# Kernel optimization log

Measured on AMD Instinct MI355X. Metric: run time of the kernel, lower is better.

## Reference

```python
import jax, jax.numpy as jnp
import numpy as np


def setup_inputs() -> dict:
    key = jax.random.key(0)
    k1, k2, k3, k4 = jax.random.split(key, 4)
    N, M, D = 4096, 4096, 1024
    H = jax.random.normal(k1, (N, D), dtype=jnp.float32)
    K = jax.random.normal(k2, (M, D), dtype=jnp.float32)
    V = jax.random.normal(k3, (M, D), dtype=jnp.float32)
    attn_mask = jax.random.uniform(k4, (N, M), dtype=jnp.float32)
    return {"H": H, "K": K, "V": V, "attn_mask": attn_mask}


def reference(H, K, V, attn_mask):
    # scores: [N, M] = H @ K^T, scaled by sqrt(d)
    d = H.shape[1]
    scores = jnp.matmul(H, K.T) / jnp.sqrt(jnp.asarray(d, dtype=H.dtype))
    # double softmax with elementwise mask multiply in between
    probs = jax.nn.softmax(jax.nn.softmax(scores, axis=1) * attn_mask, axis=1)
    return jnp.matmul(probs, V)
```

## Files before the change

kernel.cpp:

```cpp
#include <hip/hip_runtime.h>
#include <cstdint>

typedef unsigned short u16;
typedef __bf16 bf16x8 __attribute__((ext_vector_type(8)));
typedef float f32x4 __attribute__((ext_vector_type(4)));
typedef unsigned int u32x4 __attribute__((ext_vector_type(4)));

__device__ __forceinline__ float bf2f(u16 h) {
  union { unsigned int u; float f; } v; v.u = ((unsigned int)h) << 16; return v.f;
}
__device__ __forceinline__ u16 f2bf(float f) {
  union { float f; unsigned int u; } v; v.f = f;
  unsigned int u = v.u;
  return (u16)((u + 0x7FFFu + ((u >> 16) & 1u)) >> 16);
}

__device__ __forceinline__ void ld_lds16(const void* g, void* l) {
  __builtin_amdgcn_global_load_lds(
      (const __attribute__((address_space(1))) unsigned int*)g,
      (__attribute__((address_space(3))) unsigned int*)l, 16, 0, 0);
}

__global__ __launch_bounds__(512, 2) void gemm1_kernel(
    const u16* __restrict__ A, const u16* __restrict__ B,
    u16* __restrict__ S, int ldA, int ldB, int ldC)
{
  __shared__ __align__(16) u16 smem[65536];

  const int tid  = threadIdx.x;
  const int lane = tid & 63;
  const int w    = tid >> 6;
  const int wr   = w >> 2;
  const int wc   = w & 3;
  const int quad = lane >> 4;
  const int cIn  = lane & 15;
  const int lrow   = lane >> 3;
  const int gchunk = (lane & 7) ^ lrow;

  const int flat = blockIdx.x;
  const int xcd  = flat & 7;
  const int i    = flat >> 3;
  const int rowT = (xcd >> 1) * 4 + (i & 3);
  const int colT = (xcd & 1) * 8 + (i >> 2);
  const int rowBlk = rowT * 256;
  const int colBlk = colT * 256;

  f32x4 acc[8][4];
  #pragma unroll
  for (int a = 0; a < 8; ++a)
    #pragma unroll
    for (int b = 0; b < 4; ++b) acc[a][b] = {0.f, 0.f, 0.f, 0.f};

  auto stageA = [&](int buf, int kt2) {
    #pragma unroll
    for (int l = 0; l < 4; ++l) {
      const u16* ga = A + (size_t)(rowBlk + l * 64 + w * 8 + lrow) * ldA
                        + kt2 * 64 + gchunk * 8;
      ld_lds16(ga, &smem[buf * 16384 + l * 4096 + w * 512]);
    }
  };
  auto stageB = [&](int buf, int kt2) {
    #pragma unroll
    for (int l = 0; l < 4; ++l) {
      const u16* gb = B + (size_t)(colBlk + l * 64 + w * 8 + lrow) * ldB
                        + kt2 * 64 + gchunk * 8;
      ld_lds16(gb, &smem[32768 + buf * 16384 + l * 4096 + w * 512]);
    }
  };

  stageA(0, 0);
  stageB(0, 0);
  __syncthreads();

  for (int kt = 0; kt < 16; ++kt) {
    const int cur = kt & 1;
    const int aBase = cur * 16384;
    const int bBase = 32768 + cur * 16384;

    bf16x8 bf[4][2];
    #pragma unroll
    for (int q = 0; q < 4; ++q) {
      if (q == 0) {
        if (kt + 1 < 16) stageA(cur ^ 1, kt + 1);
        #pragma unroll
        for (int ni = 0; ni < 4; ++ni)
          #pragma unroll
          for (int ks = 0; ks < 2; ++ks) {
            int row = wc * 64 + ni * 16 + cIn;
            int ch  = (ks * 4 + quad) ^ (row & 7);
            bf[ni][ks] = *(const bf16x8*)&smem[bBase + row * 64 + ch * 8];
          }
      }
      if (q == 1 && kt + 1 < 16) stageB(cur ^ 1, kt + 1);

      bf16x8 af[2][2];
      #pragma unroll
      for (int m = 0; m < 2; ++m)
        #pragma unroll
        for (int ks = 0; ks < 2; ++ks) {
          int row = wr * 128 + (q * 2 + m) * 16 + cIn;
          int ch  = (ks * 4 + quad) ^ (row & 7);
          af[m][ks] = *(const bf16x8*)&smem[aBase + row * 64 + ch * 8];
        }

      __builtin_amdgcn_s_barrier();
      asm volatile("s_waitcnt lgkmcnt(0)" ::: "memory");
      __builtin_amdgcn_sched_barrier(0);
      __builtin_amdgcn_s_setprio(1);
      #pragma unroll
      for (int m = 0; m < 2; ++m)
        #pragma unroll
        for (int ni = 0; ni < 4; ++ni)
          #pragma unroll
          for (int ks = 0; ks < 2; ++ks)
            acc[q * 2 + m][ni] = __builtin_amdgcn_mfma_f32_16x16x32_bf16(
                af[m][ks], bf[ni][ks], acc[q * 2 + m][ni], 0, 0, 0);
      __builtin_amdgcn_s_setprio(0);
      __builtin_amdgcn_sched_barrier(0);
      if (q < 3) __builtin_amdgcn_s_barrier();
    }
    __syncthreads();
  }

  const float scale = 0.03125f;
  u16* epi = smem;
  #pragma unroll
  for (int R = 0; R < 4; ++R) {
    #pragma unroll
    for (int m01 = 0; m01 < 2; ++m01) {
      int mi = R * 2 + m01;
      #pragma unroll
      for (int ni = 0; ni < 4; ++ni) {
        int col = wc * 64 + ni * 16 + cIn;
        #pragma unroll
        for (int r = 0; r < 4; ++r) {
          int er = wr * 32 + m01 * 16 + quad * 4 + r;
          epi[er * 264 + col] = f2bf(acc[mi][ni][r] * scale);
        }
      }
    }
    __syncthreads();
    #pragma unroll
    for (int it = 0; it < 4; ++it) {
      int idx = it * 512 + tid;
      int er  = idx >> 5;
      int c8  = idx & 31;
      int grow = rowBlk + (er >> 5) * 128 + (R * 2 + ((er >> 4) & 1)) * 16 + (er & 15);
      u32x4 v = *(const u32x4*)&epi[er * 264 + c8 * 8];
      *(u32x4*)&S[(size_t)grow * ldC + colBlk + c8 * 8] = v;
    }
    __syncthreads();
  }
}

__global__ __launch_bounds__(256) void gemm2_kernel(
    const u16* __restrict__ A, const u16* __restrict__ B,
    float* __restrict__ Out, const float* __restrict__ L2,
    int ldA, int ldB, int ldC)
{
  __shared__ __align__(16) u16 smem[49152];

  const int tid  = threadIdx.x;
  const int lane = tid & 63;
  const int w    = tid >> 6;
  const int wrow = w >> 1;
  const int wcol = w & 1;
  const int quad = lane >> 4;
  const int cIn  = lane & 15;
  const int lrow   = lane >> 3;
  const int gchunk = (lane & 7) ^ lrow;

  const int flat = blockIdx.x;
  const int xcd  = flat & 7;
  const int i    = flat >> 3;
  const int rowBlk = (xcd * 4 + (i & 3)) * 128;
  const int colBlk = (i >> 2) * 128;

  f32x4 acc[4][4];
  #pragma unroll
  for (int a = 0; a < 4; ++a)
    #pragma unroll
    for (int b = 0; b < 4; ++b) acc[a][b] = {0.f, 0.f, 0.f, 0.f};

  auto stage = [&](int buf, int kt) {
    int kk = kt * 64;
    #pragma unroll
    for (int t = 0; t < 4; ++t) {
      int rg = w * 4 + t;
      const u16* ga = A + (size_t)(rowBlk + rg * 8 + lrow) * ldA + kk + gchunk * 8;
      ld_lds16(ga, &smem[buf * 8192 + rg * 512]);
      const u16* gb = B + (size_t)(colBlk + rg * 8 + lrow) * ldB + kk + gchunk * 8;
      ld_lds16(gb, &smem[24576 + buf * 8192 + rg * 512]);
    }
  };

  stage(0, 0);
  stage(1, 1);

  int cur = 0;
  for (int kt = 0; kt < 64; ++kt) {
    if (kt < 63) asm volatile("s_waitcnt vmcnt(8)" ::: "memory");
    else         asm volatile("s_waitcnt vmcnt(0)" ::: "memory");
    __builtin_amdgcn_s_barrier();
    __builtin_amdgcn_sched_barrier(0);

    if (kt + 2 < 64) {
      int nb = cur + 2; if (nb >= 3) nb -= 3;
      stage(nb, kt + 2);
    }

    const int aBase = cur * 8192;
    const int bBase = 24576 + cur * 8192;
    #pragma unroll
    for (int ks = 0; ks < 2; ++ks) {
      bf16x8 af[4], bfr[4];
      #pragma unroll
      for (int mi = 0; mi < 4; ++mi) {
        int row = wrow * 64 + mi * 16 + cIn;
        int ch  = (ks * 4 + quad) ^ (row & 7);
        af[mi]  = *(const bf16x8*)&smem[aBase + row * 64 + ch * 8];
      }
      #pragma unroll
      for (int ni = 0; ni < 4; ++ni) {
        int row = wcol * 64 + ni * 16 + cIn;
        int ch  = (ks * 4 + quad) ^ (row & 7);
        bfr[ni] = *(const bf16x8*)&smem[bBase + row * 64 + ch * 8];
      }
      #pragma unroll
      for (int mi = 0; mi < 4; ++mi)
        #pragma unroll
        for (int ni = 0; ni < 4; ++ni)
          acc[mi][ni] = __builtin_amdgcn_mfma_f32_16x16x32_bf16(
              af[mi], bfr[ni], acc[mi][ni], 0, 0, 0);
    }

    cur = (cur + 1 == 3) ? 0 : cur + 1;
  }

  #pragma unroll
  for (int mi = 0; mi < 4; ++mi) {
    #pragma unroll
    for (int r = 0; r < 4; ++r) {
      int row   = rowBlk + wrow * 64 + mi * 16 + quad * 4 + r;
      float inv = 1.0f / L2[row];
      #pragma unroll
      for (int ni = 0; ni < 4; ++ni) {
        int col = colBlk + wcol * 64 + ni * 16 + cIn;
        __builtin_nontemporal_store(acc[mi][ni][r] * inv,
                                    &Out[(size_t)row * ldC + col]);
      }
    }
  }
}

__global__ __launch_bounds__(256) void prep_kernel(
    const float* __restrict__ H, const float* __restrict__ Kin,
    const float* __restrict__ V, u16* __restrict__ Hb, u16* __restrict__ Kb,
    u16* __restrict__ Vt)
{
  int b = blockIdx.x;
  if (b < 8192) {
    const float* src = (b < 4096) ? H : Kin;
    u16* dst = (b < 4096) ? Hb : Kb;
    int i = (b & 4095) * 256 + threadIdx.x;
    f32x4 v = __builtin_nontemporal_load(&((const f32x4*)src)[i]);
    ushort4 o;
    o.x = f2bf(v.x); o.y = f2bf(v.y); o.z = f2bf(v.z); o.w = f2bf(v.w);
    ((ushort4*)dst)[i] = o;
  } else {
    __shared__ float tile[32][33];
    b -= 8192;
    int c0 = (b & 31) * 32;
    int r0 = (b >> 5) * 32;
    int tx = threadIdx.x & 31, ty = threadIdx.x >> 5;
    #pragma unroll
    for (int s = 0; s < 32; s += 8)
      tile[ty + s][tx] = __builtin_nontemporal_load(
          &V[(size_t)(r0 + ty + s) * 1024 + c0 + tx]);
    __syncthreads();
    #pragma unroll
    for (int s = 0; s < 32; s += 8)
      Vt[(size_t)(c0 + ty + s) * 4096 + r0 + tx] = f2bf(tile[tx][ty + s]);
  }
}

__global__ __launch_bounds__(256) void softmax2_kernel(
    u16* __restrict__ S, const float* __restrict__ mask,
    float* __restrict__ L2, int M)
{
  int row = blockIdx.x;
  u16* srow = S + (size_t)row * M;
  const float* mrow = mask + (size_t)row * M;
  const int base = threadIdx.x * 16;

  u16 sl[16];
  *(uint4*)(sl)     = *(const uint4*)(srow + base);
  *(uint4*)(sl + 8) = *(const uint4*)(srow + base + 8);

  float e[16];
  float s1 = 0.f;
  #pragma unroll
  for (int j = 0; j < 16; ++j) { e[j] = __expf(bf2f(sl[j])); s1 += e[j]; }

  __shared__ float wred[8];
  #pragma unroll
  for (int m = 1; m < 64; m <<= 1) s1 += __shfl_xor(s1, m, 64);
  if ((threadIdx.x & 63) == 0) wred[threadIdx.x >> 6] = s1;
  __syncthreads();
  float inv = 1.0f / (wred[0] + wred[1] + wred[2] + wred[3]);

  float mv[16];
  #pragma unroll
  for (int q = 0; q < 4; ++q) {
    f32x4 m4 = __builtin_nontemporal_load((const f32x4*)(mrow + base + q * 4));
    mv[q * 4 + 0] = m4.x; mv[q * 4 + 1] = m4.y;
    mv[q * 4 + 2] = m4.z; mv[q * 4 + 3] = m4.w;
  }

  float lsum = 0.f;
  #pragma unroll
  for (int j = 0; j < 16; ++j) {
    float p = __expf(e[j] * inv * mv[j]);
    lsum += p;
    sl[j] = f2bf(p);
  }
  *(uint4*)(srow + base)     = *(uint4*)(sl);
  *(uint4*)(srow + base + 8) = *(uint4*)(sl + 8);

  #pragma unroll
  for (int m = 1; m < 64; m <<= 1) lsum += __shfl_xor(lsum, m, 64);
  if ((threadIdx.x & 63) == 0) wred[4 + (threadIdx.x >> 6)] = lsum;
  __syncthreads();
  if (threadIdx.x == 0) L2[row] = wred[4] + wred[5] + wred[6] + wred[7];
}

extern "C" void kernel_launch(void* const* d_in, const int* in_sizes, int n_in,
                              void* d_out, int out_size, void* d_ws, size_t ws_size,
                              hipStream_t stream) {
  const float* H    = (const float*)d_in[0];
  const float* Kin  = (const float*)d_in[1];
  const float* V    = (const float*)d_in[2];
  const float* mask = (const float*)d_in[3];
  float* out = (float*)d_out;

  const int N = 4096, M = 4096, D = 1024;

  char* ws = (char*)d_ws;
  u16*   Hb = (u16*)(ws);
  u16*   Kb = (u16*)(ws + (8ull << 20));
  u16*   Vt = (u16*)(ws + (16ull << 20));
  u16*   S  = (u16*)(ws + (24ull << 20));
  float* L2 = (float*)(ws + (56ull << 20));

  prep_kernel<<<dim3(12288), dim3(256), 0, stream>>>(H, Kin, V, Hb, Kb, Vt);

  gemm1_kernel<<<dim3(256), dim3(512), 0, stream>>>(Hb, Kb, S, D, D, M);

  softmax2_kernel<<<dim3(N), dim3(256), 0, stream>>>(S, mask, L2, M);

  gemm2_kernel<<<dim3(256), dim3(256), 0, stream>>>(S, Vt, out, L2, M, M, D);
}
```

Baseline: 234.6 us.

## Split gemm2 K-loop across wave pairs with LDS reduction, 512 threads

gemm2 now runs 8 waves per block instead of 4. Each pair of waves splits the 64-wide K tile in half, and the two partial accumulators are combined through LDS in the epilogue. Global-to-LDS staging is spread over twice as many threads, and the MFMA section is raised in priority with s_setprio. The aim is more latency hiding and more MFMA issue per CU for the small grid of 256 blocks, at the cost of an extra LDS reduction pass and barriers.

```diff
diff --git a/kernel.cpp b/kernel.cpp
--- a/kernel.cpp
+++ b/kernel.cpp
@@ -153,7 +153,7 @@
   }
 }
 
-__global__ __launch_bounds__(256) void gemm2_kernel(
+__global__ __launch_bounds__(512, 2) void gemm2_kernel(
     const u16* __restrict__ A, const u16* __restrict__ B,
     float* __restrict__ Out, const float* __restrict__ L2,
     int ldA, int ldB, int ldC)
@@ -163,8 +163,9 @@
   const int tid  = threadIdx.x;
   const int lane = tid & 63;
   const int w    = tid >> 6;
-  const int wrow = w >> 1;
-  const int wcol = w & 1;
+  const int wk   = w & 1;
+  const int wrow = (w >> 1) & 1;
+  const int wcol = (w >> 2) & 1;
   const int quad = lane >> 4;
   const int cIn  = lane & 15;
   const int lrow   = lane >> 3;
@@ -185,8 +186,8 @@
   auto stage = [&](int buf, int kt) {
     int kk = kt * 64;
     #pragma unroll
-    for (int t = 0; t < 4; ++t) {
-      int rg = w * 4 + t;
+    for (int t = 0; t < 2; ++t) {
+      int rg = w * 2 + t;
       const u16* ga = A + (size_t)(rowBlk + rg * 8 + lrow) * ldA + kk + gchunk * 8;
       ld_lds16(ga, &smem[buf * 8192 + rg * 512]);
       const u16* gb = B + (size_t)(colBlk + rg * 8 + lrow) * ldB + kk + gchunk * 8;
@@ -199,7 +200,7 @@
 
   int cur = 0;
   for (int kt = 0; kt < 64; ++kt) {
-    if (kt < 63) asm volatile("s_waitcnt vmcnt(8)" ::: "memory");
+    if (kt < 63) asm volatile("s_waitcnt vmcnt(4)" ::: "memory");
     else         asm volatile("s_waitcnt vmcnt(0)" ::: "memory");
     __builtin_amdgcn_s_barrier();
     __builtin_amdgcn_sched_barrier(0);
@@ -211,43 +212,58 @@
 
     const int aBase = cur * 8192;
     const int bBase = 24576 + cur * 8192;
-    #pragma unroll
-    for (int ks = 0; ks < 2; ++ks) {
-      bf16x8 af[4], bfr[4];
-      #pragma unroll
-      for (int mi = 0; mi < 4; ++mi) {
-        int row = wrow * 64 + mi * 16 + cIn;
-        int ch  = (ks * 4 + quad) ^ (row & 7);
-        af[mi]  = *(const bf16x8*)&smem[aBase + row * 64 + ch * 8];
-      }
-      #pragma unroll
-      for (int ni = 0; ni < 4; ++ni) {
-        int row = wcol * 64 + ni * 16 + cIn;
-        int ch  = (ks * 4 + quad) ^ (row & 7);
-        bfr[ni] = *(const bf16x8*)&smem[bBase + row * 64 + ch * 8];
-      }
-      #pragma unroll
-      for (int mi = 0; mi < 4; ++mi)
-        #pragma unroll
-        for (int ni = 0; ni < 4; ++ni)
-          acc[mi][ni] = __builtin_amdgcn_mfma_f32_16x16x32_bf16(
-              af[mi], bfr[ni], acc[mi][ni], 0, 0, 0);
-    }
+    bf16x8 af[4], bfr[4];
+    #pragma unroll
+    for (int mi = 0; mi < 4; ++mi) {
+      int row = wrow * 64 + mi * 16 + cIn;
+      int ch  = (wk * 4 + quad) ^ (row & 7);
+      af[mi]  = *(const bf16x8*)&smem[aBase + row * 64 + ch * 8];
+    }
+    #pragma unroll
+    for (int ni = 0; ni < 4; ++ni) {
+      int row = wcol * 64 + ni * 16 + cIn;
+      int ch  = (wk * 4 + quad) ^ (row & 7);
+      bfr[ni] = *(const bf16x8*)&smem[bBase + row * 64 + ch * 8];
+    }
+    __builtin_amdgcn_s_setprio(1);
+    #pragma unroll
+    for (int mi = 0; mi < 4; ++mi)
+      #pragma unroll
+      for (int ni = 0; ni < 4; ++ni)
+        acc[mi][ni] = __builtin_amdgcn_mfma_f32_16x16x32_bf16(
+            af[mi], bfr[ni], acc[mi][ni], 0, 0, 0);
+    __builtin_amdgcn_s_setprio(0);
 
     cur = (cur + 1 == 3) ? 0 : cur + 1;
   }
 
-  #pragma unroll
-  for (int mi = 0; mi < 4; ++mi) {
-    #pragma unroll
-    for (int r = 0; r < 4; ++r) {
-      int row   = rowBlk + wrow * 64 + mi * 16 + quad * 4 + r;
-      float inv = 1.0f / L2[row];
-      #pragma unroll
-      for (int ni = 0; ni < 4; ++ni) {
-        int col = colBlk + wcol * 64 + ni * 16 + cIn;
-        __builtin_nontemporal_store(acc[mi][ni][r] * inv,
-                                    &Out[(size_t)row * ldC + col]);
+  float* red = (float*)smem;
+  const int ow = w >> 1;
+  const int rbase = ow * 4160 + lane * 65;
+  __syncthreads();
+  if (wk == 1) {
+    #pragma unroll
+    for (int mi = 0; mi < 4; ++mi)
+      #pragma unroll
+      for (int ni = 0; ni < 4; ++ni)
+        #pragma unroll
+        for (int r = 0; r < 4; ++r)
+          red[rbase + (mi * 4 + ni) * 4 + r] = acc[mi][ni][r];
+  }
+  __syncthreads();
+  if (wk == 0) {
+    #pragma unroll
+    for (int mi = 0; mi < 4; ++mi) {
+      #pragma unroll
+      for (int r = 0; r < 4; ++r) {
+        int row   = rowBlk + wrow * 64 + mi * 16 + quad * 4 + r;
+        float inv = 1.0f / L2[row];
+        #pragma unroll
+        for (int ni = 0; ni < 4; ++ni) {
+          int col = colBlk + wcol * 64 + ni * 16 + cIn;
+          float v = acc[mi][ni][r] + red[rbase + (mi * 4 + ni) * 4 + r];
+          __builtin_nontemporal_store(v * inv, &Out[(size_t)row * ldC + col]);
+        }
       }
     }
   }
@@ -358,5 +374,5 @@
 
   softmax2_kernel<<<dim3(N), dim3(256), 0, stream>>>(S, mask, L2, M);
 
-  gemm2_kernel<<<dim3(256), dim3(256), 0, stream>>>(S, Vt, out, L2, M, M, D);
-}
+  gemm2_kernel<<<dim3(256), dim3(512), 0, stream>>>(S, Vt, out, L2, M, M, D);
+}
```

New measurement: 227.5 us. -3.0%, faster.
